# Kernel optimization log

Hardware: AMD Instinct MI355X
Metric: run time of the kernel (lower is better)

## Reference

```python
import jax, jax.numpy as jnp
import numpy as np

N, D_IN, D_OUT, BATCH = 64, 512, 512, 1024


def setup_inputs() -> dict:
    key = jax.random.key(0)
    kx, kw, kb = jax.random.split(key, 3)
    x = jax.random.normal(kx, (BATCH, N, D_IN), dtype=jnp.float32)
    # nn.Linear-style init: U(-1/sqrt(d_in), 1/sqrt(d_in)); weight stored transposed (n, d_in, d_out)
    bound = 1.0 / np.sqrt(D_IN)
    weight = jax.random.uniform(kw, (N, D_IN, D_OUT), minval=-bound, maxval=bound, dtype=jnp.float32)
    bias = jax.random.uniform(kb, (N, D_OUT), minval=-bound, maxval=bound, dtype=jnp.float32)
    return {"x": x, "weight": weight, "bias": bias}


def reference(x, weight, bias):
    # Same math as (x[..., None] * weight[None]).sum(-2) + bias[None],
    # expressed as a batched GEMM over the n independent linear layers.
    out = jnp.einsum("bni,nio->bno", x, weight)  # (batch, n, d_out)
    return out + bias[None]
```

## Files before the change

### kernel.cpp

```cpp
#include <hip/hip_runtime.h>
#include <hip/hip_bf16.h>

#define NL    64
#define DIN   512
#define DOUT  512
#define BATCH 1024

#define BM 256
#define BN 256
#define BK 32
#define NK (DIN / BK)
#define LDSS 40

typedef short short8 __attribute__((ext_vector_type(8)));
typedef float f32x4  __attribute__((ext_vector_type(4)));

__device__ __forceinline__ unsigned int pk2(float a, float b) {
    __hip_bfloat162 h = __float22bfloat162_rn(make_float2(a, b));
    unsigned int r;
    __builtin_memcpy(&r, &h, 4);
    return r;
}

__global__ __launch_bounds__(512, 2) void nlinear_kernel(
        const float* __restrict__ x, const float* __restrict__ w,
        const float* __restrict__ bias, float* __restrict__ out) {
    __shared__ unsigned short As[2][BM * LDSS];
    __shared__ unsigned short Bs[2][BN * LDSS];

    const int tid = threadIdx.x;
    const int bid = blockIdx.x;
    const int nb    = (bid & 7) * 64 + (bid >> 3);
    const int layer = nb >> 3;
    const int t8    = nb & 7;
    const int bm0   = (t8 & 3) * BM;
    const int bn0   = (t8 >> 2) * BN;

    const int wid  = tid >> 6;
    const int lane = tid & 63;
    const int wr   = wid >> 2, wc = wid & 3;
    const int lrow = lane & 15;
    const int lkb  = lane >> 4;

    const int ar = tid >> 3;
    const int ak = tid & 7;
    const int gw = tid >> 6;
    const int gc = tid & 63;

    const size_t XS = (size_t)NL * DIN;
    const float* xb = x + (size_t)bm0 * XS + (size_t)layer * DIN;
    const float* wb = w + (size_t)layer * DIN * DOUT + bn0;
    const float* aptr0 = xb + (size_t)ar * XS + ak * 4;
    const float* bptr0 = wb + (size_t)(gw * 4) * DOUT + gc * 4;

    f32x4 acc[8][4];
#pragma unroll
    for (int i = 0; i < 8; ++i)
#pragma unroll
        for (int j = 0; j < 4; ++j) acc[i][j] = (f32x4){0.f, 0.f, 0.f, 0.f};

    f32x4 avE[4], avO[4];
    f32x4 bv[4];

    auto issueA = [&](int kt, f32x4 (&s)[4]) {
#pragma unroll
        for (int p = 0; p < 4; ++p)
            s[p] = *reinterpret_cast<const f32x4*>(
                aptr0 + (size_t)(64 * p) * XS + kt * BK);
    };
    auto issueB = [&](int kt) {
#pragma unroll
        for (int p = 0; p < 4; ++p)
            bv[p] = *reinterpret_cast<const f32x4*>(
                bptr0 + (size_t)(kt * BK + p) * DOUT);
    };

    auto cvtwriteA = [&](int db, f32x4 (&s)[4]) {
#pragma unroll
        for (int p = 0; p < 4; ++p) {
            uint2 wv;
            wv.x = pk2(s[p][0], s[p][1]);
            wv.y = pk2(s[p][2], s[p][3]);
            *reinterpret_cast<uint2*>(
                &As[db][(ar + 64 * p) * LDSS + ak * 4]) = wv;
        }
    };
    auto cvtwriteB = [&](int db) {
#pragma unroll
        for (int j = 0; j < 4; ++j) {
            const int c = gc * 4 + j;
            uint2 wv;
            wv.x = pk2(bv[0][j], bv[1][j]);
            wv.y = pk2(bv[2][j], bv[3][j]);
            const int slot = gw ^ ((c >> 2) & 7);
            *reinterpret_cast<uint2*>(
                &Bs[db][c * LDSS + slot * 4]) = wv;
        }
    };

    auto fragA = [&](int db, short8* af) {
#pragma unroll
        for (int mi = 0; mi < 8; ++mi) {
            const int row = wr * 128 + mi * 16 + lrow;
            af[mi] = *reinterpret_cast<const short8*>(
                &As[db][row * LDSS + lkb * 8]);
        }
    };
    auto fragB = [&](int db, short8* bf) {
#pragma unroll
        for (int ni = 0; ni < 4; ++ni) {
            const int col = wc * 64 + ni * 16 + lrow;
            const int key = (col >> 2) & 7;
            const unsigned short* base = &Bs[db][col * LDSS];
            uint2 lo = *reinterpret_cast<const uint2*>(
                base + (((2 * lkb) ^ key) << 2));
            uint2 hi = *reinterpret_cast<const uint2*>(
                base + (((2 * lkb + 1) ^ key) << 2));
            uint4 u = make_uint4(lo.x, lo.y, hi.x, hi.y);
            __builtin_memcpy(&bf[ni], &u, 16);
        }
    };

#define BARRIER() do { \
        asm volatile("s_waitcnt lgkmcnt(0)" ::: "memory"); \
        __builtin_amdgcn_sched_barrier(0); \
        __builtin_amdgcn_s_barrier(); \
        __builtin_amdgcn_sched_barrier(0); } while (0)

#define COMPUTE(DB, AF, BF) do { \
        fragA(DB, AF); \
        fragB(DB, BF); \
        asm volatile("s_waitcnt lgkmcnt(0)" ::: "memory"); \
        __builtin_amdgcn_sched_barrier(0); \
        __builtin_amdgcn_s_setprio(1); \
        _Pragma("unroll") \
        for (int mi = 0; mi < 8; ++mi) \
        _Pragma("unroll") \
            for (int ni = 0; ni < 4; ++ni) \
                acc[mi][ni] = __builtin_amdgcn_mfma_f32_16x16x32_bf16( \
                    AF[mi], BF[ni], acc[mi][ni], 0, 0, 0); \
        __builtin_amdgcn_s_setprio(0); \
        __builtin_amdgcn_sched_barrier(0); } while (0)

    issueA(0, avE);
    issueB(0);
    cvtwriteA(0, avE);
    cvtwriteB(0);
    issueA(1, avO);
    issueB(1);
    issueA(2, avE);
    BARRIER();

#pragma unroll 1
    for (int k = 0; k < NK - 2; k += 2) {
        {
            short8 af[8], bf[4];
            COMPUTE(0, af, bf);
            cvtwriteA(1, avO);
            cvtwriteB(1);
            issueA(k + 3, avO);
            issueB(k + 2);
            BARRIER();
        }
        {
            short8 af[8], bf[4];
            COMPUTE(1, af, bf);
            cvtwriteA(0, avE);
            cvtwriteB(0);
            if (k + 4 < NK) issueA(k + 4, avE);
            issueB(k + 3);
            BARRIER();
        }
    }
    {
        short8 af[8], bf[4];
        COMPUTE(0, af, bf);
        cvtwriteA(1, avO);
        cvtwriteB(1);
        BARRIER();
    }
    {
        short8 af[8], bf[4];
        COMPUTE(1, af, bf);
    }

    const float* bb = bias + (size_t)layer * DOUT + bn0;
    float* ob = out + (size_t)bm0 * (NL * DOUT) + (size_t)layer * DOUT + bn0;
#pragma unroll
    for (int mi = 0; mi < 8; ++mi) {
#pragma unroll
        for (int ni = 0; ni < 4; ++ni) {
            const int col = wc * 64 + ni * 16 + lrow;
            const float bval = bb[col];
#pragma unroll
            for (int r = 0; r < 4; ++r) {
                const int row = wr * 128 + mi * 16 + lkb * 4 + r;
                ob[(size_t)row * (NL * DOUT) + col] = acc[mi][ni][r] + bval;
            }
        }
    }
#undef BARRIER
#undef COMPUTE
}

extern "C" void kernel_launch(void* const* d_in, const int* in_sizes, int n_in,
                              void* d_out, int out_size, void* d_ws, size_t ws_size,
                              hipStream_t stream) {
    const float* x  = (const float*)d_in[0];
    const float* w  = (const float*)d_in[1];
    const float* b  = (const float*)d_in[2];
    float* out      = (float*)d_out;

    dim3 grid(NL * (BATCH / BM) * (DOUT / BN));
    dim3 block(512);
    hipLaunchKernelGGL(nlinear_kernel, grid, block, 0, stream, x, w, b, out);
}
```

Baseline: 94.44 us.

## Stage full x row-panel in LDS with 64x512 tiles, stream weights only

Changes tiling to 64-row by full-512-column output tiles per block. The entire bf16-converted x panel (64x512) is loaded once into swizzled dynamic LDS, and only the weight tiles are double-buffered through the k loop. This removes the per-step A load/convert work and the duplicate reads of x across column tiles. In exchange, weights are re-read more often, LDS use rises to about 144KB (one block per CU), each wave's MFMA work per k-step halves, and the A preload is not overlapped with compute.

```diff
diff --git a/kernel.cpp b/kernel.cpp
--- a/kernel.cpp
+++ b/kernel.cpp
@@ -6,11 +6,13 @@
 #define DOUT  512
 #define BATCH 1024
 
-#define BM 256
-#define BN 256
+#define BM 64
+#define BN 512
 #define BK 32
 #define NK (DIN / BK)
-#define LDSS 40
+#define BLDSS 40
+#define ASH (BM * DIN)
+#define BSH (BN * BLDSS)
 
 typedef short short8 __attribute__((ext_vector_type(8)));
 typedef float f32x4  __attribute__((ext_vector_type(4)));
@@ -22,96 +24,80 @@
     return r;
 }
 
-__global__ __launch_bounds__(512, 2) void nlinear_kernel(
+__global__ __launch_bounds__(512) void nlinear_kernel(
         const float* __restrict__ x, const float* __restrict__ w,
         const float* __restrict__ bias, float* __restrict__ out) {
-    __shared__ unsigned short As[2][BM * LDSS];
-    __shared__ unsigned short Bs[2][BN * LDSS];
+    extern __shared__ unsigned short lds[];
+    unsigned short* const Asm = lds;
+    unsigned short* const Bsm = lds + ASH;
 
     const int tid = threadIdx.x;
     const int bid = blockIdx.x;
-    const int nb    = (bid & 7) * 64 + (bid >> 3);
-    const int layer = nb >> 3;
-    const int t8    = nb & 7;
-    const int bm0   = (t8 & 3) * BM;
-    const int bn0   = (t8 >> 2) * BN;
-
-    const int wid  = tid >> 6;
+    const int nb    = (bid & 7) * 128 + (bid >> 3);
+    const int layer = nb >> 4;
+    const int bm0   = (nb & 15) * BM;
+
     const int lane = tid & 63;
-    const int wr   = wid >> 2, wc = wid & 3;
+    const int wc   = tid >> 6;
     const int lrow = lane & 15;
     const int lkb  = lane >> 4;
 
-    const int ar = tid >> 3;
-    const int ak = tid & 7;
+    const int arow = tid >> 3;
+    const int ac8  = tid & 7;
     const int gw = tid >> 6;
     const int gc = tid & 63;
 
     const size_t XS = (size_t)NL * DIN;
-    const float* xb = x + (size_t)bm0 * XS + (size_t)layer * DIN;
-    const float* wb = w + (size_t)layer * DIN * DOUT + bn0;
-    const float* aptr0 = xb + (size_t)ar * XS + ak * 4;
-    const float* bptr0 = wb + (size_t)(gw * 4) * DOUT + gc * 4;
-
-    f32x4 acc[8][4];
-#pragma unroll
-    for (int i = 0; i < 8; ++i)
+    const float* aptr = x + (size_t)(bm0 + arow) * XS + (size_t)layer * DIN;
+    const float* wb   = w + (size_t)layer * DIN * DOUT;
+    const float* bptr = wb + (size_t)(gw * 4) * DOUT + gc * 8;
+
+    f32x4 acc[4][4];
+#pragma unroll
+    for (int i = 0; i < 4; ++i)
 #pragma unroll
         for (int j = 0; j < 4; ++j) acc[i][j] = (f32x4){0.f, 0.f, 0.f, 0.f};
 
-    f32x4 avE[4], avO[4];
-    f32x4 bv[4];
-
-    auto issueA = [&](int kt, f32x4 (&s)[4]) {
-#pragma unroll
-        for (int p = 0; p < 4; ++p)
-            s[p] = *reinterpret_cast<const f32x4*>(
-                aptr0 + (size_t)(64 * p) * XS + kt * BK);
-    };
-    auto issueB = [&](int kt) {
-#pragma unroll
-        for (int p = 0; p < 4; ++p)
-            bv[p] = *reinterpret_cast<const f32x4*>(
-                bptr0 + (size_t)(kt * BK + p) * DOUT);
-    };
-
-    auto cvtwriteA = [&](int db, f32x4 (&s)[4]) {
-#pragma unroll
-        for (int p = 0; p < 4; ++p) {
+    f32x4 bvr[4][2];
+
+    auto issueB = [&](int t) {
+#pragma unroll
+        for (int ki = 0; ki < 4; ++ki) {
+            const float* p = bptr + (size_t)(t * BK + ki) * DOUT;
+            bvr[ki][0] = *reinterpret_cast<const f32x4*>(p);
+            bvr[ki][1] = *reinterpret_cast<const f32x4*>(p + 4);
+        }
+    };
+    auto cvtwriteB = [&](int db) {
+        unsigned short* dst = Bsm + db * BSH;
+#pragma unroll
+        for (int j = 0; j < 8; ++j) {
+            const int c = gc * 8 + j;
+            const int h = j >> 2, e = j & 3;
             uint2 wv;
-            wv.x = pk2(s[p][0], s[p][1]);
-            wv.y = pk2(s[p][2], s[p][3]);
-            *reinterpret_cast<uint2*>(
-                &As[db][(ar + 64 * p) * LDSS + ak * 4]) = wv;
-        }
-    };
-    auto cvtwriteB = [&](int db) {
-#pragma unroll
-        for (int j = 0; j < 4; ++j) {
-            const int c = gc * 4 + j;
-            uint2 wv;
-            wv.x = pk2(bv[0][j], bv[1][j]);
-            wv.y = pk2(bv[2][j], bv[3][j]);
+            wv.x = pk2(bvr[0][h][e], bvr[1][h][e]);
+            wv.y = pk2(bvr[2][h][e], bvr[3][h][e]);
             const int slot = gw ^ ((c >> 2) & 7);
-            *reinterpret_cast<uint2*>(
-                &Bs[db][c * LDSS + slot * 4]) = wv;
-        }
-    };
-
-    auto fragA = [&](int db, short8* af) {
-#pragma unroll
-        for (int mi = 0; mi < 8; ++mi) {
-            const int row = wr * 128 + mi * 16 + lrow;
+            *reinterpret_cast<uint2*>(&dst[c * BLDSS + slot * 4]) = wv;
+        }
+    };
+
+    auto fragA = [&](int t, short8* af) {
+#pragma unroll
+        for (int mi = 0; mi < 4; ++mi) {
+            const int row = mi * 16 + lrow;
+            const int s   = t * 4 + lkb;
             af[mi] = *reinterpret_cast<const short8*>(
-                &As[db][row * LDSS + lkb * 8]);
+                &Asm[row * DIN + ((s ^ (row & 7)) << 3)]);
         }
     };
     auto fragB = [&](int db, short8* bf) {
+        const unsigned short* src = Bsm + db * BSH;
 #pragma unroll
         for (int ni = 0; ni < 4; ++ni) {
             const int col = wc * 64 + ni * 16 + lrow;
             const int key = (col >> 2) & 7;
-            const unsigned short* base = &Bs[db][col * LDSS];
+            const unsigned short* base = &src[col * BLDSS];
             uint2 lo = *reinterpret_cast<const uint2*>(
                 base + (((2 * lkb) ^ key) << 2));
             uint2 hi = *reinterpret_cast<const uint2*>(
@@ -127,74 +113,70 @@
         __builtin_amdgcn_s_barrier(); \
         __builtin_amdgcn_sched_barrier(0); } while (0)
 
-#define COMPUTE(DB, AF, BF) do { \
-        fragA(DB, AF); \
-        fragB(DB, BF); \
+#define COMPUTE(T, DB) do { \
+        short8 af[4], bf[4]; \
+        fragA(T, af); \
+        fragB(DB, bf); \
         asm volatile("s_waitcnt lgkmcnt(0)" ::: "memory"); \
         __builtin_amdgcn_sched_barrier(0); \
         __builtin_amdgcn_s_setprio(1); \
         _Pragma("unroll") \
-        for (int mi = 0; mi < 8; ++mi) \
+        for (int mi = 0; mi < 4; ++mi) \
         _Pragma("unroll") \
             for (int ni = 0; ni < 4; ++ni) \
                 acc[mi][ni] = __builtin_amdgcn_mfma_f32_16x16x32_bf16( \
-                    AF[mi], BF[ni], acc[mi][ni], 0, 0, 0); \
+                    af[mi], bf[ni], acc[mi][ni], 0, 0, 0); \
         __builtin_amdgcn_s_setprio(0); \
         __builtin_amdgcn_sched_barrier(0); } while (0)
 
-    issueA(0, avE);
     issueB(0);
-    cvtwriteA(0, avE);
+    {
+#pragma unroll
+        for (int i = 0; i < 8; ++i) {
+            const float* p = aptr + i * 64 + ac8 * 8;
+            f32x4 v0 = *reinterpret_cast<const f32x4*>(p);
+            f32x4 v1 = *reinterpret_cast<const f32x4*>(p + 4);
+            uint4 wv;
+            wv.x = pk2(v0[0], v0[1]);
+            wv.y = pk2(v0[2], v0[3]);
+            wv.z = pk2(v1[0], v1[1]);
+            wv.w = pk2(v1[2], v1[3]);
+            const int s = i * 8 + ac8;
+            *reinterpret_cast<uint4*>(
+                &Asm[arow * DIN + ((s ^ (arow & 7)) << 3)]) = wv;
+        }
+    }
     cvtwriteB(0);
-    issueA(1, avO);
     issueB(1);
-    issueA(2, avE);
     BARRIER();
 
 #pragma unroll 1
-    for (int k = 0; k < NK - 2; k += 2) {
-        {
-            short8 af[8], bf[4];
-            COMPUTE(0, af, bf);
-            cvtwriteA(1, avO);
-            cvtwriteB(1);
-            issueA(k + 3, avO);
-            issueB(k + 2);
-            BARRIER();
-        }
-        {
-            short8 af[8], bf[4];
-            COMPUTE(1, af, bf);
-            cvtwriteA(0, avE);
-            cvtwriteB(0);
-            if (k + 4 < NK) issueA(k + 4, avE);
-            issueB(k + 3);
-            BARRIER();
-        }
+    for (int t = 0; t < NK - 2; ++t) {
+        COMPUTE(t, t & 1);
+        cvtwriteB((t + 1) & 1);
+        issueB(t + 2);
+        BARRIER();
     }
     {
-        short8 af[8], bf[4];
-        COMPUTE(0, af, bf);
-        cvtwriteA(1, avO);
-        cvtwriteB(1);
+        COMPUTE(NK - 2, (NK - 2) & 1);
+        cvtwriteB((NK - 1) & 1);
         BARRIER();
     }
     {
-        short8 af[8], bf[4];
-        COMPUTE(1, af, bf);
-    }
-
-    const float* bb = bias + (size_t)layer * DOUT + bn0;
-    float* ob = out + (size_t)bm0 * (NL * DOUT) + (size_t)layer * DOUT + bn0;
-#pragma unroll
-    for (int mi = 0; mi < 8; ++mi) {
+        COMPUTE(NK - 1, (NK - 1) & 1);
+    }
+
+    const float* bb = bias + (size_t)layer * DOUT;
+    float* ob = out + (size_t)bm0 * (NL * DOUT) + (size_t)layer * DOUT;
+#pragma unroll
+    for (int mi = 0; mi < 4; ++mi) {
 #pragma unroll
         for (int ni = 0; ni < 4; ++ni) {
             const int col = wc * 64 + ni * 16 + lrow;
             const float bval = bb[col];
 #pragma unroll
             for (int r = 0; r < 4; ++r) {
-                const int row = wr * 128 + mi * 16 + lkb * 4 + r;
+                const int row = mi * 16 + lkb * 4 + r;
                 ob[(size_t)row * (NL * DOUT) + col] = acc[mi][ni][r] + bval;
             }
         }
@@ -211,7 +193,12 @@
     const float* b  = (const float*)d_in[2];
     float* out      = (float*)d_out;
 
-    dim3 grid(NL * (BATCH / BM) * (DOUT / BN));
+    const int lds_bytes = (ASH + 2 * BSH) * 2;
+    hipFuncSetAttribute((const void*)nlinear_kernel,
+                        hipFuncAttributeMaxDynamicSharedMemorySize, lds_bytes);
+
+    dim3 grid(NL * (BATCH / BM));
     dim3 block(512);
-    hipLaunchKernelGGL(nlinear_kernel, grid, block, 0, stream, x, w, b, out);
+    hipLaunchKernelGGL(nlinear_kernel, grid, block, lds_bytes, stream,
+                       x, w, b, out);
 }
```

Result: slower. 166.4 us (+76.2%).
